# Optimization experiments

Hardware: AMD Instinct MI355X
Metric: run time of the kernel (lower is better)

The kernel has to match this reference:

```python
import jax, jax.numpy as jnp
import numpy as np

CH = 512
HEADS = 8
GROUPS = 8
EPS = 1e-5


def setup_inputs() -> dict:
    key = jax.random.key(0)
    ks = jax.random.split(key, 7)
    B, C, H, W = 8, CH, 32, 32
    s_in = 1.0 / np.sqrt(C)
    return {
        "x": jax.random.normal(ks[0], (B, C, H, W), dtype=jnp.float32),
        "gn_w": jnp.ones((C,), dtype=jnp.float32),
        "gn_b": jnp.zeros((C,), dtype=jnp.float32),
        "qkv_w": jax.random.normal(ks[1], (3 * C, C), dtype=jnp.float32) * s_in,
        "qkv_b": jnp.zeros((3 * C,), dtype=jnp.float32),
        "proj_w": jax.random.normal(ks[2], (C, C), dtype=jnp.float32) * s_in,
        "proj_b": jnp.zeros((C,), dtype=jnp.float32),
    }


def reference(x, gn_w, gn_b, qkv_w, qkv_b, proj_w, proj_b):
    B, C, H, W = x.shape
    d = C // HEADS
    # GroupNorm(8, C): normalize over (C/G, H, W) within each group
    xg = x.reshape(B, GROUPS, C // GROUPS, H, W)
    mu = jnp.mean(xg, axis=(2, 3, 4), keepdims=True)
    var = jnp.var(xg, axis=(2, 3, 4), keepdims=True)
    xn = ((xg - mu) * jax.lax.rsqrt(var + EPS)).reshape(B, C, H, W)
    xn = xn * gn_w[None, :, None, None] + gn_b[None, :, None, None]
    # 1x1 conv QKV -> (B, 3C, H, W)
    qkv = jnp.einsum('bchw,oc->bohw', xn, qkv_w) + qkv_b[None, :, None, None]
    # (B,3,heads,d,HW) -> (3,B,heads,HW,d)
    qkv = qkv.reshape(B, 3, HEADS, d, H * W).transpose(1, 0, 2, 4, 3)
    q, k, v = qkv[0], qkv[1], qkv[2]
    scale = d ** (-0.5)
    attn = jax.nn.softmax(jnp.einsum('bhnd,bhmd->bhnm', q, k) * scale, axis=-1)
    out = jnp.einsum('bhnm,bhmd->bhnd', attn, v)  # (B,heads,HW,d)
    out = out.transpose(0, 1, 3, 2).reshape(B, C, H, W)
    out = jnp.einsum('bchw,oc->bohw', out, proj_w) + proj_b[None, :, None, None]
    return out + x
```

## Files before the change

### kernel.cpp

```cpp
#include <hip/hip_runtime.h>

typedef float        f32x4 __attribute__((ext_vector_type(4)));
typedef unsigned int u32x4 __attribute__((ext_vector_type(4)));
typedef unsigned short u16;

#define NB   8
#define NC   512
#define NHW  1024
#define NHEAD 8
#define ND   64

__device__ __forceinline__ u16 f2bf(float f) {
    unsigned u = __builtin_bit_cast(unsigned, f);
    u += 0x7fffu + ((u >> 16) & 1u);
    return (u16)(u >> 16);
}

__device__ __forceinline__ void MFMA(f32x4& d, u32x4 a, u32x4 b) {
    asm("v_mfma_f32_16x16x32_bf16 %0, %1, %2, %0" : "+v"(d) : "v"(a), "v"(b));
}

__device__ __forceinline__ unsigned cvtpk_bf16(float lo, float hi) {
    unsigned r;
    asm("v_cvt_pk_bf16_f32 %0, %1, %2" : "=v"(r) : "v"(lo), "v"(hi));
    return r;
}

__device__ __forceinline__ void gload_lds16(const void* g, void* l) {
    __builtin_amdgcn_global_load_lds(
        (const __attribute__((address_space(1))) unsigned int*)g,
        (__attribute__((address_space(3))) unsigned int*)l, 16, 0, 0);
}

__global__ void k_prep(const float* __restrict__ x, float* __restrict__ stats,
                       const float* __restrict__ qkvw, u16* __restrict__ wqb,
                       const float* __restrict__ pwt,  u16* __restrict__ wpb) {
    const int blk = blockIdx.x;
    if (blk < 64) {
        const float4* p = (const float4*)(x + (size_t)blk * 65536);
        float s = 0.f, ss = 0.f;
        for (int i = threadIdx.x; i < 16384; i += 256) {
            float4 v = p[i];
            s  += v.x + v.y + v.z + v.w;
            ss += v.x*v.x + v.y*v.y + v.z*v.z + v.w*v.w;
        }
        #pragma unroll
        for (int m = 32; m >= 1; m >>= 1) { s += __shfl_xor(s, m); ss += __shfl_xor(ss, m); }
        __shared__ float ls[4], lss[4];
        const int w = threadIdx.x >> 6;
        if ((threadIdx.x & 63) == 0) { ls[w] = s; lss[w] = ss; }
        __syncthreads();
        if (threadIdx.x == 0) {
            float S = ls[0]+ls[1]+ls[2]+ls[3], SS = lss[0]+lss[1]+lss[2]+lss[3];
            float mu  = S * (1.f/65536.f);
            float var = SS * (1.f/65536.f) - mu*mu;
            ((float2*)stats)[blk] = make_float2(mu, rsqrtf(var + 1e-5f));
        }
    } else {
        int i = (blk - 64) * 256 + threadIdx.x;
        const float* in; u16* out;
        if (i < 196608) { in = qkvw; out = wqb; }
        else            { in = pwt;  out = wpb; i -= 196608; }
        float4 v = ((const float4*)in)[i];
        ((ushort4*)out)[i] = make_ushort4(f2bf(v.x), f2bf(v.y), f2bf(v.z), f2bf(v.w));
    }
}

__global__ void k_normt(const float* __restrict__ x, const float* __restrict__ gw,
                        const float* __restrict__ gb, const float* __restrict__ stats,
                        u16* __restrict__ xnt) {
    const int cb = blockIdx.x, nb = blockIdx.y, b = blockIdx.z;
    __shared__ float t[64][65];
    const float2 st = ((const float2*)stats)[b*8 + cb];
    const int tx = threadIdx.x & 15, ty = threadIdx.x >> 4;
    const float* xb = x + ((size_t)(b*NC + cb*64))*NHW + nb*64;
    #pragma unroll
    for (int i = 0; i < 4; ++i) {
        int c = ty + i*16;
        float a  = st.y * gw[cb*64 + c];
        float bb = gb[cb*64 + c] - st.x * a;
        float4 v = *(const float4*)(xb + (size_t)c*NHW + tx*4);
        t[c][tx*4+0] = v.x*a + bb;
        t[c][tx*4+1] = v.y*a + bb;
        t[c][tx*4+2] = v.z*a + bb;
        t[c][tx*4+3] = v.w*a + bb;
    }
    __syncthreads();
    u16* ob = xnt + ((size_t)(b*NHW + nb*64))*NC + cb*64;
    #pragma unroll
    for (int i = 0; i < 4; ++i) {
        int n = ty + i*16, c0 = tx*4;
        *(ushort4*)(ob + (size_t)n*NC + c0) =
            make_ushort4(f2bf(t[c0][n]), f2bf(t[c0+1][n]), f2bf(t[c0+2][n]), f2bf(t[c0+3][n]));
    }
}

__device__ __forceinline__ void gemm_core(const u16* __restrict__ A, const u16* __restrict__ Bm,
                                          int Mb, size_t nrowbase,
                                          u16* Asm_, u16* Bsm_, f32x4 (&acc)[4][4]) {
    const int tid = threadIdx.x, wave = tid >> 6, lane = tid & 63;
    const int l15 = lane & 15, l4 = lane >> 4;
    const int wr = wave >> 1, wc = wave & 1;

    auto stage = [&](int kt, int buf) {
        u16* Ab = Asm_ + buf*8192;
        u16* Bb = Bsm_ + buf*8192;
        #pragma unroll
        for (int i = 0; i < 4; ++i) {
            int li  = wave*4 + i;
            int p   = li*64 + lane;
            int row = p >> 3;
            int lc  = (p & 7) ^ (row & 7);
            gload_lds16(A  + (((size_t)(Mb + row)) << 9) + kt*64 + lc*8, Ab + li*512);
            gload_lds16(Bm + ((nrowbase + row)      << 9) + kt*64 + lc*8, Bb + li*512);
        }
    };

    stage(0, 0);
    asm volatile("s_waitcnt vmcnt(0)" ::: "memory");
    __syncthreads();

    for (int kt = 0; kt < 8; ++kt) {
        const int cur = kt & 1;
        if (kt < 7) stage(kt + 1, cur ^ 1);
        const u16* Ab = Asm_ + cur*8192;
        const u16* Bb = Bsm_ + cur*8192;
        u32x4 af[4][2], bf[4][2];
        #pragma unroll
        for (int mt = 0; mt < 4; ++mt)
            #pragma unroll
            for (int ks = 0; ks < 2; ++ks) {
                int ra = wr*64 + mt*16 + l15;
                af[mt][ks] = *(const u32x4*)(Ab + ra*64 + (((l4 + ks*4) ^ (ra & 7)) << 3));
                int rb = wc*64 + mt*16 + l15;
                bf[mt][ks] = *(const u32x4*)(Bb + rb*64 + (((l4 + ks*4) ^ (rb & 7)) << 3));
            }
        __builtin_amdgcn_s_setprio(1);
        #pragma unroll
        for (int mt = 0; mt < 4; ++mt)
            #pragma unroll
            for (int nt = 0; nt < 4; ++nt)
                #pragma unroll
                for (int ks = 0; ks < 2; ++ks)
                    MFMA(acc[mt][nt], af[mt][ks], bf[nt][ks]);
        __builtin_amdgcn_s_setprio(0);
        asm volatile("s_waitcnt vmcnt(0)" ::: "memory");
        __syncthreads();
    }
}

__global__ __launch_bounds__(256, 2)
void k_gemm_qkv(const u16* __restrict__ wq, const u16* __restrict__ xnt,
                const float* __restrict__ qkvb,
                u16* __restrict__ qb, u16* __restrict__ kb, u16* __restrict__ vtb) {
    __shared__ u16 Asm_[2*128*64], Bsm_[2*128*64];
    f32x4 acc[4][4] = {};
    const int f = blockIdx.x + blockIdx.y*12 + blockIdx.z*96;
    const int pair = f & 63;
    const int Mb  = (f >> 6) * 128;
    const int Nbl = (pair & 7) * 128;
    const int b   = pair >> 3;
    gemm_core(wq, xnt, Mb, (size_t)(b*NHW + Nbl), Asm_, Bsm_, acc);
    const int tid = threadIdx.x, wave = tid >> 6, lane = tid & 63;
    const int l15 = lane & 15, l4 = lane >> 4;
    const int wr = wave >> 1, wc = wave & 1;
    const float SCL2 = 0.125f * 1.44269504088896f;
    #pragma unroll
    for (int mt = 0; mt < 4; ++mt) {
        int ob = Mb + wr*64 + mt*16 + l4*4;
        float4 bi = *(const float4*)(qkvb + ob);
        int t = ob >> 9, oc = ob & 511;
        int hh = oc >> 6, di = oc & 63;
        size_t bh = (size_t)(b*8 + hh);
        float qs = (t == 0) ? SCL2 : 1.f;
        #pragma unroll
        for (int nt = 0; nt < 4; ++nt) {
            int n = Nbl + wc*64 + nt*16 + l15;
            f32x4 a = acc[mt][nt];
            u16 e0 = f2bf((a[0] + bi.x) * qs), e1 = f2bf((a[1] + bi.y) * qs);
            u16 e2 = f2bf((a[2] + bi.z) * qs), e3 = f2bf((a[3] + bi.w) * qs);
            if (t == 0) {
                *(ushort4*)(qb + ((bh*NHW + n)*ND + di)) = make_ushort4(e0, e1, e2, e3);
            } else if (t == 1) {
                *(ushort4*)(kb + ((bh*NHW + n)*ND + di)) = make_ushort4(e0, e1, e2, e3);
            } else {
                u16* p = vtb + ((bh*ND + di)*NHW + n);
                p[0] = e0; p[1024] = e1; p[2048] = e2; p[3072] = e3;
            }
        }
    }
}

__global__ __launch_bounds__(256, 2)
void k_attn(const u16* __restrict__ qg, const u16* __restrict__ kg,
            const u16* __restrict__ vg, u16* __restrict__ og) {
    __shared__ u16 Ksm[2*64*64], Vsm[2*64*64], Psm[4*32*64];
    const int f = blockIdx.x + (blockIdx.y << 3) + (blockIdx.z << 6);
    const int qt = f >> 6;
    const int pair = f & 63;
    const int h = pair & 7, b = pair >> 3;
    const int tid = threadIdx.x, wave = tid >> 6, lane = tid & 63;
    const int l15 = lane & 15, l4 = lane >> 4;
    const size_t bh = (size_t)(b*8 + h);

    auto stage = [&](int kv, int bufi) {
        u16* Kb = Ksm + bufi*4096;
        u16* Vb = Vsm + bufi*4096;
        #pragma unroll
        for (int i = 0; i < 2; ++i) {
            int li = wave*2 + i;
            int p = li*64 + lane;
            int row = p >> 3;
            int lc = (p & 7) ^ (row & 7);
            gload_lds16(kg + (bh*NHW + kv*64 + row)*ND + lc*8, Kb + li*512);
            gload_lds16(vg + (bh*ND + row)*NHW + kv*64 + lc*8, Vb + li*512);
        }
    };

    stage(0, 0);

    const int q0 = qt*128 + wave*32;
    u32x4 qf[2][2];
    #pragma unroll
    for (int mt = 0; mt < 2; ++mt) {
        const u16* qp = qg + (bh*NHW + q0 + mt*16 + l15)*ND + l4*8;
        qf[mt][0] = *(const u32x4*)(qp);
        qf[mt][1] = *(const u32x4*)(qp + 32);
    }
    f32x4 acc[4][2] = {};
    float lrun[2] = {0.f, 0.f};

    asm volatile("s_waitcnt vmcnt(0)" ::: "memory");
    __syncthreads();

    u16* pw = Psm + wave*2048;
    const int psw = (l15 & 7) << 1;

    for (int kv = 0; kv < 16; ++kv) {
        const int cur = kv & 1;
        if (kv < 15) stage(kv + 1, cur ^ 1);
        const u16* Kb = Ksm + cur*4096;
        const u16* Vb = Vsm + cur*4096;

        f32x4 sT[4][2];
        __builtin_amdgcn_s_setprio(1);
        #pragma unroll
        for (int ct = 0; ct < 4; ++ct) {
            int m = ct*16 + l15;
            u32x4 kf0 = *(const u32x4*)(Kb + m*64 + ((l4 ^ (m & 7)) << 3));
            u32x4 kf1 = *(const u32x4*)(Kb + m*64 + (((l4 + 4) ^ (m & 7)) << 3));
            #pragma unroll
            for (int mt = 0; mt < 2; ++mt) {
                f32x4 z = {-20.f, -20.f, -20.f, -20.f};
                MFMA(z, kf0, qf[mt][0]);
                MFMA(z, kf1, qf[mt][1]);
                sT[ct][mt] = z;
            }
        }
        __builtin_amdgcn_s_setprio(0);
        #pragma unroll
        for (int mt = 0; mt < 2; ++mt) {
            float rs = 0.f;
            int prow = mt*16 + l15;
            #pragma unroll
            for (int ct = 0; ct < 4; ++ct) {
                float p0 = __builtin_amdgcn_exp2f(sT[ct][mt][0]);
                float p1 = __builtin_amdgcn_exp2f(sT[ct][mt][1]);
                float p2 = __builtin_amdgcn_exp2f(sT[ct][mt][2]);
                float p3 = __builtin_amdgcn_exp2f(sT[ct][mt][3]);
                rs += (p0 + p1) + (p2 + p3);
                unsigned lo = cvtpk_bf16(p0, p1);
                unsigned hi = cvtpk_bf16(p2, p3);
                int chunk = (ct*4 + l4) ^ psw;
                *(uint2*)(pw + prow*64 + chunk*4) = make_uint2(lo, hi);
            }
            lrun[mt] += rs;
        }
        asm volatile("s_waitcnt lgkmcnt(0)" ::: "memory");
        __builtin_amdgcn_sched_barrier(0);
        u32x4 pf[2][2];
        #pragma unroll
        for (int mt = 0; mt < 2; ++mt)
            #pragma unroll
            for (int ks = 0; ks < 2; ++ks) {
                int c0 = (ks*8 + l4*2) ^ psw;
                pf[mt][ks] = *(const u32x4*)(pw + (mt*16 + l15)*64 + c0*4);
            }
        __builtin_amdgcn_s_setprio(1);
        #pragma unroll
        for (int dt = 0; dt < 4; ++dt) {
            int m = dt*16 + l15;
            u32x4 vf0 = *(const u32x4*)(Vb + m*64 + ((l4 ^ (m & 7)) << 3));
            u32x4 vf1 = *(const u32x4*)(Vb + m*64 + (((l4 + 4) ^ (m & 7)) << 3));
            #pragma unroll
            for (int mt = 0; mt < 2; ++mt) {
                MFMA(acc[dt][mt], vf0, pf[mt][0]);
                MFMA(acc[dt][mt], vf1, pf[mt][1]);
            }
        }
        __builtin_amdgcn_s_setprio(0);
        asm volatile("s_waitcnt vmcnt(0)" ::: "memory");
        __syncthreads();
    }
    float inv[2];
    #pragma unroll
    for (int mt = 0; mt < 2; ++mt) {
        float l = lrun[mt];
        l += __shfl_xor(l, 16);
        l += __shfl_xor(l, 32);
        inv[mt] = 1.f / l;
    }
    #pragma unroll
    for (int dt = 0; dt < 4; ++dt)
        #pragma unroll
        for (int mt = 0; mt < 2; ++mt) {
            int q = q0 + mt*16 + l15;
            int d = dt*16 + l4*4;
            f32x4 a = acc[dt][mt];
            *(ushort4*)(og + (size_t)(b*NHW + q)*NC + h*ND + d) =
                make_ushort4(f2bf(a[0]*inv[mt]), f2bf(a[1]*inv[mt]),
                             f2bf(a[2]*inv[mt]), f2bf(a[3]*inv[mt]));
        }
}

__global__ __launch_bounds__(256, 2)
void k_gemm_proj(const u16* __restrict__ wp, const u16* __restrict__ att,
                 const float* __restrict__ pb, const float* __restrict__ x,
                 float* __restrict__ out) {
    __shared__ u16 Asm_[2*128*64], Bsm_[2*128*64];
    f32x4 acc[4][4] = {};
    const int f = blockIdx.x + (blockIdx.y << 2) + (blockIdx.z << 5);
    const int pair = f & 63;
    const int Mb  = (f >> 6) * 128;
    const int Nbl = (pair & 7) * 128;
    const int b   = pair >> 3;
    gemm_core(wp, att, Mb, (size_t)(b*NHW + Nbl), Asm_, Bsm_, acc);
    const int tid = threadIdx.x, wave = tid >> 6, lane = tid & 63;
    const int l15 = lane & 15, l4 = lane >> 4;
    const int wr = wave >> 1, wc = wave & 1;
    #pragma unroll
    for (int mt = 0; mt < 4; ++mt) {
        int ob = Mb + wr*64 + mt*16 + l4*4;
        float4 bi = *(const float4*)(pb + ob);
        #pragma unroll
        for (int nt = 0; nt < 4; ++nt) {
            int n = Nbl + wc*64 + nt*16 + l15;
            size_t base = ((size_t)(b*NC + ob))*NHW + n;
            out[base]        = acc[mt][nt][0] + bi.x + x[base];
            out[base + 1024] = acc[mt][nt][1] + bi.y + x[base + 1024];
            out[base + 2048] = acc[mt][nt][2] + bi.z + x[base + 2048];
            out[base + 3072] = acc[mt][nt][3] + bi.w + x[base + 3072];
        }
    }
}

extern "C" void kernel_launch(void* const* d_in, const int* in_sizes, int n_in,
                              void* d_out, int out_size, void* d_ws, size_t ws_size,
                              hipStream_t stream) {
    (void)in_sizes; (void)n_in; (void)out_size; (void)ws_size;
    const float* x    = (const float*)d_in[0];
    const float* gw   = (const float*)d_in[1];
    const float* gb   = (const float*)d_in[2];
    const float* qkvw = (const float*)d_in[3];
    const float* qkvb = (const float*)d_in[4];
    const float* pw   = (const float*)d_in[5];
    const float* pbv  = (const float*)d_in[6];
    float* out = (float*)d_out;
    char* ws = (char*)d_ws;

    constexpr size_t oWQ  = 1024;
    constexpr size_t oWP  = oWQ  + (size_t)1536*512*2;
    constexpr size_t oXNT = oWP  + (size_t)512*512*2;
    constexpr size_t oQ   = oXNT + (size_t)NB*NHW*NC*2;
    constexpr size_t oK   = oQ   + (size_t)NB*NHEAD*NHW*ND*2;
    constexpr size_t oVT  = oK   + (size_t)NB*NHEAD*NHW*ND*2;

    float* stats = (float*)ws;
    u16* wqb = (u16*)(ws + oWQ);
    u16* wpb = (u16*)(ws + oWP);
    u16* xnt = (u16*)(ws + oXNT);
    u16* qb  = (u16*)(ws + oQ);
    u16* kb  = (u16*)(ws + oK);
    u16* vtb = (u16*)(ws + oVT);
    u16* att = xnt;

    k_prep<<<1088, 256, 0, stream>>>(x, stats, qkvw, wqb, pw, wpb);
    k_normt<<<dim3(8,16,8), 256, 0, stream>>>(x, gw, gb, stats, xnt);
    k_gemm_qkv<<<dim3(12,8,8), 256, 0, stream>>>(wqb, xnt, qkvb, qb, kb, vtb);
    k_attn<<<dim3(8,8,8), 256, 0, stream>>>(qb, kb, vtb, att);
    k_gemm_proj<<<dim3(4,8,8), 256, 0, stream>>>(wpb, att, pbv, x, out);
}
```

Baseline: 97.47 us.

## Load K/V tiles directly from global into registers, dropping LDS staging

```diff
diff --git a/kernel.cpp b/kernel.cpp
--- a/kernel.cpp
+++ b/kernel.cpp
@@ -194,7 +194,7 @@
 __global__ __launch_bounds__(256, 2)
 void k_attn(const u16* __restrict__ qg, const u16* __restrict__ kg,
             const u16* __restrict__ vg, u16* __restrict__ og) {
-    __shared__ u16 Ksm[2*64*64], Vsm[2*64*64], Psm[4*32*64];
+    __shared__ u16 Psm[4*32*64];
     const int f = blockIdx.x + (blockIdx.y << 3) + (blockIdx.z << 6);
     const int qt = f >> 6;
     const int pair = f & 63;
@@ -203,21 +203,8 @@
     const int l15 = lane & 15, l4 = lane >> 4;
     const size_t bh = (size_t)(b*8 + h);
 
-    auto stage = [&](int kv, int bufi) {
-        u16* Kb = Ksm + bufi*4096;
-        u16* Vb = Vsm + bufi*4096;
-        #pragma unroll
-        for (int i = 0; i < 2; ++i) {
-            int li = wave*2 + i;
-            int p = li*64 + lane;
-            int row = p >> 3;
-            int lc = (p & 7) ^ (row & 7);
-            gload_lds16(kg + (bh*NHW + kv*64 + row)*ND + lc*8, Kb + li*512);
-            gload_lds16(vg + (bh*ND + row)*NHW + kv*64 + lc*8, Vb + li*512);
-        }
-    };
-
-    stage(0, 0);
+    const u16* kbase = kg + bh*NHW*ND;
+    const u16* vbase = vg + bh*ND*NHW;
 
     const int q0 = qt*128 + wave*32;
     u32x4 qf[2][2];
@@ -230,52 +217,92 @@
     f32x4 acc[4][2] = {};
     float lrun[2] = {0.f, 0.f};
 
-    asm volatile("s_waitcnt vmcnt(0)" ::: "memory");
-    __syncthreads();
-
     u16* pw = Psm + wave*2048;
     const int psw = (l15 & 7) << 1;
 
+    u32x4 kf[4][2];
+    #pragma unroll
+    for (int ct = 0; ct < 4; ++ct) {
+        const u16* r = kbase + (ct*16 + l15)*ND + l4*8;
+        kf[ct][0] = *(const u32x4*)(r);
+        kf[ct][1] = *(const u32x4*)(r + 32);
+    }
+
     for (int kv = 0; kv < 16; ++kv) {
-        const int cur = kv & 1;
-        if (kv < 15) stage(kv + 1, cur ^ 1);
-        const u16* Kb = Ksm + cur*4096;
-        const u16* Vb = Vsm + cur*4096;
+        u32x4 vf[4][2];
+        #pragma unroll
+        for (int dt = 0; dt < 4; ++dt) {
+            const u16* r = vbase + (size_t)(dt*16 + l15)*NHW + kv*64 + l4*8;
+            vf[dt][0] = *(const u32x4*)(r);
+            vf[dt][1] = *(const u32x4*)(r + 32);
+        }
 
         f32x4 sT[4][2];
         __builtin_amdgcn_s_setprio(1);
         #pragma unroll
-        for (int ct = 0; ct < 4; ++ct) {
-            int m = ct*16 + l15;
-            u32x4 kf0 = *(const u32x4*)(Kb + m*64 + ((l4 ^ (m & 7)) << 3));
-            u32x4 kf1 = *(const u32x4*)(Kb + m*64 + (((l4 + 4) ^ (m & 7)) << 3));
+        for (int ct = 0; ct < 4; ++ct)
             #pragma unroll
             for (int mt = 0; mt < 2; ++mt) {
                 f32x4 z = {-20.f, -20.f, -20.f, -20.f};
-                MFMA(z, kf0, qf[mt][0]);
-                MFMA(z, kf1, qf[mt][1]);
+                MFMA(z, kf[ct][0], qf[mt][0]);
+                MFMA(z, kf[ct][1], qf[mt][1]);
                 sT[ct][mt] = z;
             }
-        }
         __builtin_amdgcn_s_setprio(0);
-        #pragma unroll
-        for (int mt = 0; mt < 2; ++mt) {
-            float rs = 0.f;
-            int prow = mt*16 + l15;
+
+        if (kv < 15) {
+            const u16* knext = kbase + (kv + 1)*64*ND;
+            u32x4 kfn[4][2];
             #pragma unroll
             for (int ct = 0; ct < 4; ++ct) {
-                float p0 = __builtin_amdgcn_exp2f(sT[ct][mt][0]);
-                float p1 = __builtin_amdgcn_exp2f(sT[ct][mt][1]);
-                float p2 = __builtin_amdgcn_exp2f(sT[ct][mt][2]);
-                float p3 = __builtin_amdgcn_exp2f(sT[ct][mt][3]);
-                rs += (p0 + p1) + (p2 + p3);
-                unsigned lo = cvtpk_bf16(p0, p1);
-                unsigned hi = cvtpk_bf16(p2, p3);
-                int chunk = (ct*4 + l4) ^ psw;
-                *(uint2*)(pw + prow*64 + chunk*4) = make_uint2(lo, hi);
-            }
-            lrun[mt] += rs;
-        }
+                const u16* r = knext + (ct*16 + l15)*ND + l4*8;
+                kfn[ct][0] = *(const u32x4*)(r);
+                kfn[ct][1] = *(const u32x4*)(r + 32);
+            }
+            #pragma unroll
+            for (int mt = 0; mt < 2; ++mt) {
+                float rs = 0.f;
+                int prow = mt*16 + l15;
+                #pragma unroll
+                for (int ct = 0; ct < 4; ++ct) {
+                    float p0 = __builtin_amdgcn_exp2f(sT[ct][mt][0]);
+                    float p1 = __builtin_amdgcn_exp2f(sT[ct][mt][1]);
+                    float p2 = __builtin_amdgcn_exp2f(sT[ct][mt][2]);
+                    float p3 = __builtin_amdgcn_exp2f(sT[ct][mt][3]);
+                    rs += (p0 + p1) + (p2 + p3);
+                    unsigned lo = cvtpk_bf16(p0, p1);
+                    unsigned hi = cvtpk_bf16(p2, p3);
+                    int chunk = (ct*4 + l4) ^ psw;
+                    *(uint2*)(pw + prow*64 + chunk*4) = make_uint2(lo, hi);
+                }
+                lrun[mt] += rs;
+            }
+            #pragma unroll
+            for (int ct = 0; ct < 4; ++ct) {
+                kf[ct][0] = kfn[ct][0];
+                kf[ct][1] = kfn[ct][1];
+            }
+        } else {
+            #pragma unroll
+            for (int mt = 0; mt < 2; ++mt) {
+                float rs = 0.f;
+                int prow = mt*16 + l15;
+                #pragma unroll
+                for (int ct = 0; ct < 4; ++ct) {
+                    float p0 = __builtin_amdgcn_exp2f(sT[ct][mt][0]);
+                    float p1 = __builtin_amdgcn_exp2f(sT[ct][mt][1]);
+                    float p2 = __builtin_amdgcn_exp2f(sT[ct][mt][2]);
+                    float p3 = __builtin_amdgcn_exp2f(sT[ct][mt][3]);
+                    rs += (p0 + p1) + (p2 + p3);
+                    unsigned lo = cvtpk_bf16(p0, p1);
+                    unsigned hi = cvtpk_bf16(p2, p3);
+                    int chunk = (ct*4 + l4) ^ psw;
+                    *(uint2*)(pw + prow*64 + chunk*4) = make_uint2(lo, hi);
+                }
+                lrun[mt] += rs;
+            }
+        }
+
         asm volatile("s_waitcnt lgkmcnt(0)" ::: "memory");
         __builtin_amdgcn_sched_barrier(0);
         u32x4 pf[2][2];
@@ -288,19 +315,13 @@
             }
         __builtin_amdgcn_s_setprio(1);
         #pragma unroll
-        for (int dt = 0; dt < 4; ++dt) {
-            int m = dt*16 + l15;
-            u32x4 vf0 = *(const u32x4*)(Vb + m*64 + ((l4 ^ (m & 7)) << 3));
-            u32x4 vf1 = *(const u32x4*)(Vb + m*64 + (((l4 + 4) ^ (m & 7)) << 3));
+        for (int dt = 0; dt < 4; ++dt)
             #pragma unroll
             for (int mt = 0; mt < 2; ++mt) {
-                MFMA(acc[dt][mt], vf0, pf[mt][0]);
-                MFMA(acc[dt][mt], vf1, pf[mt][1]);
-            }
-        }
+                MFMA(acc[dt][mt], vf[dt][0], pf[mt][0]);
+                MFMA(acc[dt][mt], vf[dt][1], pf[mt][1]);
+            }
         __builtin_amdgcn_s_setprio(0);
-        asm volatile("s_waitcnt vmcnt(0)" ::: "memory");
-        __syncthreads();
     }
     float inv[2];
     #pragma unroll
```

Measured after the change: 131.5 us. 1.35x slower.
